# Kernel optimization log

Measured on AMD Instinct MI355X. Metric: run time of the kernel, lower is better.

The kernel has to match this reference:

```python
import jax, jax.numpy as jnp
import numpy as np

LOOKUP_WINDOW = 101
OUTPUT_DIM = 128
NUM_BINS = 512


def setup_inputs() -> dict:
    key = jax.random.key(0)
    k1, k2 = jax.random.split(key)
    frames = jax.random.randint(k1, (16, 100, 27, 48, 3), 0, 256, dtype=jnp.int32)
    fc_w = jax.random.normal(k2, (LOOKUP_WINDOW, OUTPUT_DIM), dtype=jnp.float32) * 0.05
    fc_b = jnp.zeros((OUTPUT_DIM,), dtype=jnp.float32)
    return {"frames": frames, "fc_w": fc_w, "fc_b": fc_b}


def _color_histograms(frames):
    # frames: [B, T, H, W, 3] int32 in [0, 256)
    B, T, H, W, C = frames.shape
    f = frames.reshape(B * T, H * W, 3)
    R, G, Bc = f[:, :, 0], f[:, :, 1], f[:, :, 2]
    # 3 bits per channel -> 512 bins
    bins = ((R >> 5) << 6) + ((G >> 5) << 3) + (Bc >> 5)  # [BT, HW]
    frame_prefix = (jnp.arange(B * T, dtype=jnp.int32) << 9)[:, None]
    ids = (bins + frame_prefix).reshape(-1)
    hist = jax.ops.segment_sum(
        jnp.ones_like(ids, dtype=jnp.int32), ids,
        num_segments=B * T * NUM_BINS)
    hist = hist.reshape(B, T, NUM_BINS).astype(jnp.float32)
    # L2-normalize each frame's histogram
    hist = hist / jnp.linalg.norm(hist, axis=2, keepdims=True)
    return hist


def reference(frames, fc_w, fc_b):
    B, T = frames.shape[0], frames.shape[1]
    x = _color_histograms(frames)                  # [B, T, 512]
    sim = jnp.einsum('btd,bsd->bts', x, x)         # [B, T, T]
    half = (LOOKUP_WINDOW - 1) // 2
    padded = jnp.pad(sim, ((0, 0), (0, 0), (half, half)))  # [B, T, T+lw-1]
    # banded gather: band[b, t, w] = padded[b, t, t + w]
    idx = jnp.arange(T)[:, None] + jnp.arange(LOOKUP_WINDOW)[None, :]  # [T, lw]
    band = jnp.take_along_axis(
        padded, jnp.broadcast_to(idx[None], (B, T, LOOKUP_WINDOW)), axis=2)
    # Dense + relu
    return jax.nn.relu(band @ fc_w + fc_b)         # [B, T, 128]
```

## Files before the change

kernel.cpp:

```cpp
#include <hip/hip_runtime.h>
#include <hip/hip_bf16.h>
#include <math.h>

#define B_DIM 16
#define T_DIM 100
#define TPAD 112
#define HW_PIX (27 * 48)
#define NBINS 512
#define WIN 101
#define HALF 50
#define ODIM 128
#define NCHUNK 7
#define SSTR 132

typedef __attribute__((ext_vector_type(8))) short s16x8;
typedef __attribute__((ext_vector_type(4))) float f32x4;

__global__ __launch_bounds__(256) void hist_kernel(
    const int* __restrict__ frames, __hip_bfloat16* __restrict__ X16) {
  const int bid = blockIdx.x;
  const int tid = threadIdx.x;

  if (bid >= B_DIM * T_DIM) {
    const int pid = bid - B_DIM * T_DIM;
    const int b = pid / (TPAD - T_DIM);
    const int r = pid - b * (TPAD - T_DIM);
    unsigned int* row = (unsigned int*)(X16 + ((size_t)(b * TPAD + T_DIM + r)) * NBINS);
    row[tid] = 0u;
    return;
  }

  __shared__ int h[NBINS];
  __shared__ float red[16];

  for (int i = tid; i < NBINS; i += 256) h[i] = 0;
  __syncthreads();

  const int* fp = frames + (size_t)bid * (HW_PIX * 3);
  for (int i = tid; i < HW_PIX / 4; i += 256) {
    const int4* q = (const int4*)(fp + 12 * i);
    int4 a = q[0], c = q[1], e = q[2];
    int b0 = ((a.x >> 5) << 6) + ((a.y >> 5) << 3) + (a.z >> 5);
    int b1 = ((a.w >> 5) << 6) + ((c.x >> 5) << 3) + (c.y >> 5);
    int b2 = ((c.z >> 5) << 6) + ((c.w >> 5) << 3) + (e.x >> 5);
    int b3 = ((e.y >> 5) << 6) + ((e.z >> 5) << 3) + (e.w >> 5);
    atomicAdd(&h[b0], 1);
    atomicAdd(&h[b1], 1);
    atomicAdd(&h[b2], 1);
    atomicAdd(&h[b3], 1);
  }
  __syncthreads();

  float ss = 0.f;
  for (int i = tid; i < NBINS; i += 256) {
    float v = (float)h[i];
    ss += v * v;
  }
  const int lane = tid & 63, wave = tid >> 6;
#pragma unroll
  for (int off = 32; off > 0; off >>= 1) ss += __shfl_down(ss, off);
  if (lane == 0) red[wave] = ss;
  __syncthreads();
  if (tid == 0) red[8] = 1.0f / sqrtf(red[0] + red[1] + red[2] + red[3]);
  __syncthreads();
  const float rn = red[8];

  const int b = bid / T_DIM;
  const int t = bid - b * T_DIM;
  __hip_bfloat16* row = X16 + ((size_t)(b * TPAD + t)) * NBINS;
  for (int i = tid; i < NBINS; i += 256) row[i] = __float2bfloat16((float)h[i] * rn);
}

__global__ __launch_bounds__(256) void simband_fc_kernel(
    const __hip_bfloat16* __restrict__ X16, const float* __restrict__ fc_w,
    const float* __restrict__ fc_b, float* __restrict__ out) {
  __shared__ __align__(16) float wlds[WIN * ODIM];
  __shared__ float slds[16 * SSTR];

  const int cid = blockIdx.x;
  const int b = cid / NCHUNK;
  const int t0 = (cid - b * NCHUNK) * 16;
  const int s0 = t0 - HALF;
  const int tid = threadIdx.x;
  const int lane = tid & 63, w = tid >> 6;
  const int m16 = lane & 15, quad = lane >> 4;

  {
    const f32x4* src = (const f32x4*)fc_w;
    f32x4* dst = (f32x4*)wlds;
    for (int i = tid; i < (WIN * ODIM) / 4; i += 256) dst[i] = src[i];
  }

  {
    const int c0 = 2 * w;
    const short* A = (const short*)(X16 + ((size_t)(b * TPAD + t0 + m16)) * NBINS) + quad * 8;
    int sa = s0 + c0 * 16 + m16;
    int sb = sa + 16;
    sa = min(max(sa, 0), TPAD - 1);
    sb = min(max(sb, 0), TPAD - 1);
    const short* B0 = (const short*)(X16 + ((size_t)(b * TPAD + sa)) * NBINS) + quad * 8;
    const short* B1 = (const short*)(X16 + ((size_t)(b * TPAD + sb)) * NBINS) + quad * 8;

    f32x4 acc0 = {0.f, 0.f, 0.f, 0.f};
    f32x4 acc1 = {0.f, 0.f, 0.f, 0.f};
#pragma unroll 4
    for (int k = 0; k < NBINS; k += 32) {
      s16x8 af = *(const s16x8*)(A + k);
      acc0 = __builtin_amdgcn_mfma_f32_16x16x32_bf16(af, *(const s16x8*)(B0 + k), acc0, 0, 0, 0);
      acc1 = __builtin_amdgcn_mfma_f32_16x16x32_bf16(af, *(const s16x8*)(B1 + k), acc1, 0, 0, 0);
    }
#pragma unroll
    for (int r = 0; r < 4; ++r) {
      slds[(quad * 4 + r) * SSTR + c0 * 16 + m16] = acc0[r];
      slds[(quad * 4 + r) * SSTR + (c0 + 1) * 16 + m16] = acc1[r];
    }
  }
  __syncthreads();

  const int g4 = tid & 31;
  const int tl0 = tid >> 5;
  const int tl1 = tl0 + 8;
  const int t_a = t0 + tl0, t_b = t0 + tl1;
  const int jlo0 = max(0, HALF - t_a), jhi0 = min(WIN, HALF + T_DIM - t_a);
  const int jlo1 = max(0, HALF - t_b), jhi1 = min(WIN, HALF + T_DIM - t_b);

  f32x4 acc0 = ((const f32x4*)fc_b)[g4];
  f32x4 acc1 = acc0;
#pragma unroll 4
  for (int j = 0; j < WIN; ++j) {
    f32x4 wv = *(const f32x4*)&wlds[j * ODIM + g4 * 4];
    float b0 = (j >= jlo0 && j < jhi0) ? slds[tl0 * SSTR + tl0 + j] : 0.f;
    float b1 = (j >= jlo1 && j < jhi1) ? slds[tl1 * SSTR + tl1 + j] : 0.f;
    acc0 += wv * b0;
    acc1 += wv * b1;
  }

#pragma unroll
  for (int c = 0; c < 4; ++c) {
    acc0[c] = fmaxf(acc0[c], 0.f);
    acc1[c] = fmaxf(acc1[c], 0.f);
  }

  if (t_a < T_DIM)
    *(f32x4*)&out[(((size_t)b * T_DIM + t_a)) * ODIM + g4 * 4] = acc0;
  if (t_b < T_DIM)
    *(f32x4*)&out[(((size_t)b * T_DIM + t_b)) * ODIM + g4 * 4] = acc1;
}

extern "C" void kernel_launch(void* const* d_in, const int* in_sizes, int n_in,
                              void* d_out, int out_size, void* d_ws, size_t ws_size,
                              hipStream_t stream) {
  const int* frames = (const int*)d_in[0];
  const float* fc_w = (const float*)d_in[1];
  const float* fc_b = (const float*)d_in[2];
  float* out = (float*)d_out;

  __hip_bfloat16* X16 = (__hip_bfloat16*)d_ws;

  hist_kernel<<<B_DIM * T_DIM + B_DIM * (TPAD - T_DIM), 256, 0, stream>>>(frames, X16);
  simband_fc_kernel<<<B_DIM * NCHUNK, 256, 0, stream>>>(X16, fc_w, fc_b, out);
}
```

Before: 89.60 us.

## Fuse histogram and sim-band FC kernels into one cooperative kernel with grid sync

Merges the two launches into a single cooperative kernel. Each of 448 blocks builds histograms for four frames in turn, then a grid-wide sync precedes the banded similarity and FC stage on the first 112 blocks. This removes one launch and the gap between kernels, at the cost of each block handling four histograms serially and the overhead of a grid barrier. The shared-memory union is large (about 60 KB), which limits occupancy during the histogram phase.

```diff
diff --git a/kernel.cpp b/kernel.cpp
--- a/kernel.cpp
+++ b/kernel.cpp
@@ -1,6 +1,9 @@
 #include <hip/hip_runtime.h>
 #include <hip/hip_bf16.h>
+#include <hip/hip_cooperative_groups.h>
 #include <math.h>
+
+namespace cg = cooperative_groups;
 
 #define B_DIM 16
 #define T_DIM 100
@@ -12,77 +15,90 @@
 #define ODIM 128
 #define NCHUNK 7
 #define SSTR 132
+#define NUNITS (B_DIM * T_DIM + B_DIM * (TPAD - T_DIM))
+#define GRID_BLOCKS 448
 
 typedef __attribute__((ext_vector_type(8))) short s16x8;
 typedef __attribute__((ext_vector_type(4))) float f32x4;
 
-__global__ __launch_bounds__(256) void hist_kernel(
-    const int* __restrict__ frames, __hip_bfloat16* __restrict__ X16) {
-  const int bid = blockIdx.x;
+__global__ __launch_bounds__(256) void fused_kernel(
+    const int* __restrict__ frames, const float* __restrict__ fc_w,
+    const float* __restrict__ fc_b, float* __restrict__ out,
+    __hip_bfloat16* __restrict__ X16) {
+  __shared__ __align__(16) char smem[WIN * ODIM * 4 + 16 * SSTR * 4];
+
   const int tid = threadIdx.x;
+  const int lane = tid & 63, w = tid >> 6;
 
-  if (bid >= B_DIM * T_DIM) {
-    const int pid = bid - B_DIM * T_DIM;
-    const int b = pid / (TPAD - T_DIM);
-    const int r = pid - b * (TPAD - T_DIM);
-    unsigned int* row = (unsigned int*)(X16 + ((size_t)(b * TPAD + T_DIM + r)) * NBINS);
-    row[tid] = 0u;
-    return;
+  {
+    int* h = (int*)smem;
+    float* red = (float*)(smem + NBINS * 4);
+
+#pragma unroll 1
+    for (int i = 0; i < 4; ++i) {
+      const int u = blockIdx.x * 4 + i;
+      if (u >= B_DIM * T_DIM) {
+        const int pid = u - B_DIM * T_DIM;
+        const int b = pid / (TPAD - T_DIM);
+        const int r = pid - b * (TPAD - T_DIM);
+        unsigned int* row = (unsigned int*)(X16 + ((size_t)(b * TPAD + T_DIM + r)) * NBINS);
+        row[tid] = 0u;
+        continue;
+      }
+
+      for (int k = tid; k < NBINS; k += 256) h[k] = 0;
+      __syncthreads();
+
+      const int* fp = frames + (size_t)u * (HW_PIX * 3);
+      for (int g = tid; g < HW_PIX / 4; g += 256) {
+        const int4* q = (const int4*)(fp + 12 * g);
+        int4 a = q[0], c = q[1], e = q[2];
+        int b0 = ((a.x >> 5) << 6) + ((a.y >> 5) << 3) + (a.z >> 5);
+        int b1 = ((a.w >> 5) << 6) + ((c.x >> 5) << 3) + (c.y >> 5);
+        int b2 = ((c.z >> 5) << 6) + ((c.w >> 5) << 3) + (e.x >> 5);
+        int b3 = ((e.y >> 5) << 6) + ((e.z >> 5) << 3) + (e.w >> 5);
+        atomicAdd(&h[b0], 1);
+        atomicAdd(&h[b1], 1);
+        atomicAdd(&h[b2], 1);
+        atomicAdd(&h[b3], 1);
+      }
+      __syncthreads();
+
+      float ss = 0.f;
+      for (int k = tid; k < NBINS; k += 256) {
+        float v = (float)h[k];
+        ss += v * v;
+      }
+#pragma unroll
+      for (int off = 32; off > 0; off >>= 1) ss += __shfl_down(ss, off);
+      if (lane == 0) red[w] = ss;
+      __syncthreads();
+      if (tid == 0) red[8] = 1.0f / sqrtf(red[0] + red[1] + red[2] + red[3]);
+      __syncthreads();
+      const float rn = red[8];
+
+      const int b = u / T_DIM;
+      const int t = u - b * T_DIM;
+      __hip_bfloat16* row = X16 + ((size_t)(b * TPAD + t)) * NBINS;
+      __hip_bfloat162 v2;
+      v2.x = __float2bfloat16((float)h[2 * tid] * rn);
+      v2.y = __float2bfloat16((float)h[2 * tid + 1] * rn);
+      ((__hip_bfloat162*)row)[tid] = v2;
+      __syncthreads();
+    }
   }
 
-  __shared__ int h[NBINS];
-  __shared__ float red[16];
+  cg::this_grid().sync();
 
-  for (int i = tid; i < NBINS; i += 256) h[i] = 0;
-  __syncthreads();
+  if (blockIdx.x >= B_DIM * NCHUNK) return;
 
-  const int* fp = frames + (size_t)bid * (HW_PIX * 3);
-  for (int i = tid; i < HW_PIX / 4; i += 256) {
-    const int4* q = (const int4*)(fp + 12 * i);
-    int4 a = q[0], c = q[1], e = q[2];
-    int b0 = ((a.x >> 5) << 6) + ((a.y >> 5) << 3) + (a.z >> 5);
-    int b1 = ((a.w >> 5) << 6) + ((c.x >> 5) << 3) + (c.y >> 5);
-    int b2 = ((c.z >> 5) << 6) + ((c.w >> 5) << 3) + (e.x >> 5);
-    int b3 = ((e.y >> 5) << 6) + ((e.z >> 5) << 3) + (e.w >> 5);
-    atomicAdd(&h[b0], 1);
-    atomicAdd(&h[b1], 1);
-    atomicAdd(&h[b2], 1);
-    atomicAdd(&h[b3], 1);
-  }
-  __syncthreads();
-
-  float ss = 0.f;
-  for (int i = tid; i < NBINS; i += 256) {
-    float v = (float)h[i];
-    ss += v * v;
-  }
-  const int lane = tid & 63, wave = tid >> 6;
-#pragma unroll
-  for (int off = 32; off > 0; off >>= 1) ss += __shfl_down(ss, off);
-  if (lane == 0) red[wave] = ss;
-  __syncthreads();
-  if (tid == 0) red[8] = 1.0f / sqrtf(red[0] + red[1] + red[2] + red[3]);
-  __syncthreads();
-  const float rn = red[8];
-
-  const int b = bid / T_DIM;
-  const int t = bid - b * T_DIM;
-  __hip_bfloat16* row = X16 + ((size_t)(b * TPAD + t)) * NBINS;
-  for (int i = tid; i < NBINS; i += 256) row[i] = __float2bfloat16((float)h[i] * rn);
-}
-
-__global__ __launch_bounds__(256) void simband_fc_kernel(
-    const __hip_bfloat16* __restrict__ X16, const float* __restrict__ fc_w,
-    const float* __restrict__ fc_b, float* __restrict__ out) {
-  __shared__ __align__(16) float wlds[WIN * ODIM];
-  __shared__ float slds[16 * SSTR];
+  float* wlds = (float*)smem;
+  float* slds = (float*)(smem + WIN * ODIM * 4);
 
   const int cid = blockIdx.x;
   const int b = cid / NCHUNK;
   const int t0 = (cid - b * NCHUNK) * 16;
   const int s0 = t0 - HALF;
-  const int tid = threadIdx.x;
-  const int lane = tid & 63, w = tid >> 6;
   const int m16 = lane & 15, quad = lane >> 4;
 
   {
@@ -154,9 +170,9 @@
   const float* fc_w = (const float*)d_in[1];
   const float* fc_b = (const float*)d_in[2];
   float* out = (float*)d_out;
-
   __hip_bfloat16* X16 = (__hip_bfloat16*)d_ws;
 
-  hist_kernel<<<B_DIM * T_DIM + B_DIM * (TPAD - T_DIM), 256, 0, stream>>>(frames, X16);
-  simband_fc_kernel<<<B_DIM * NCHUNK, 256, 0, stream>>>(X16, fc_w, fc_b, out);
+  void* args[] = {(void*)&frames, (void*)&fc_w, (void*)&fc_b, (void*)&out, (void*)&X16};
+  hipLaunchCooperativeKernel((const void*)fused_kernel, dim3(GRID_BLOCKS), dim3(256),
+                             args, 0, stream);
 }
```

New measurement: 154.5 us. 1.72x slower.
